# Kernel optimization log

Measured on AMD Instinct MI355X. Metric: run time of the kernel, lower is better.

## Reference

```python
import jax, jax.numpy as jnp
import numpy as np

N = 100000   # total nodes in batch
E = 200000   # total edges
G = 4000     # number of graphs
H = 128      # gin_size = gin_hidden = gin_mlp_hidden = linear_hidden
L = 2        # gin_layers


def setup_inputs() -> dict:
    key = jax.random.key(0)
    ks = jax.random.split(key, 24)
    rn = lambda i, shape, s=0.05: (jax.random.normal(ks[i], shape, jnp.float32) * s)
    inp = dict(
        x=rn(0, (N, 14), 1.0),
        edge_attr=rn(1, (E, 4), 1.0),
        edge_index=jax.random.randint(ks[2], (2, E), 0, N, dtype=jnp.int32),
        batch=jnp.sort(jax.random.randint(ks[3], (N,), 0, G, dtype=jnp.int32)),
        node_w=rn(4, (14, H)), node_b=jnp.zeros((H,), jnp.float32),
        edge_w=rn(5, (4, H)), edge_b=jnp.zeros((H,), jnp.float32),
        eps=jnp.zeros((L,), jnp.float32),
        gin_w1=rn(6, (L, H, H)), gin_b1=jnp.zeros((L, H), jnp.float32),
        gin_w2=rn(7, (L, H, H)), gin_b2=jnp.zeros((L, H), jnp.float32),
        em_w1=rn(8, (L, H, H)), em_b1=jnp.zeros((L, H), jnp.float32),
        em_w2=rn(9, (L, H, H)), em_b2=jnp.zeros((L, H), jnp.float32),
        gru_wih=rn(10, (3 * H, H)), gru_whh=rn(11, (3 * H, H)),
        gru_bih=jnp.zeros((3 * H,), jnp.float32), gru_bhh=jnp.zeros((3 * H,), jnp.float32),
        lstm_wih=rn(12, (4 * H, 2 * H)), lstm_whh=rn(13, (4 * H, H)),
        lstm_bih=jnp.zeros((4 * H,), jnp.float32), lstm_bhh=jnp.zeros((4 * H,), jnp.float32),
        fc_w1=rn(14, (2 * H, H)), fc_b1=jnp.zeros((H,), jnp.float32),
        fc_w2=rn(15, (H, 1)), fc_b2=jnp.zeros((1,), jnp.float32),
    )
    return inp


def reference(x, edge_attr, edge_index, batch,
              node_w, node_b, edge_w, edge_b, eps,
              gin_w1, gin_b1, gin_w2, gin_b2,
              em_w1, em_b1, em_w2, em_b2,
              gru_wih, gru_whh, gru_bih, gru_bhh,
              lstm_wih, lstm_whh, lstm_bih, lstm_bhh,
              fc_w1, fc_b1, fc_w2, fc_b2):
    src, dst = edge_index[0], edge_index[1]
    node = x @ node_w + node_b          # [N,H]
    edge = edge_attr @ edge_w + edge_b  # [E,H]
    h = node                            # GRU hidden state
    for l in range(L):
        # GINEConv: msg = relu(x_src + e), scatter-add to dst, (1+eps)*x + agg, then MLP
        msg = jax.nn.relu(node[src] + edge)                     # [E,H] gather
        agg = jax.ops.segment_sum(msg, dst, num_segments=N)     # [N,H] scatter-add
        z = (1.0 + eps[l]) * node + agg
        m = jax.nn.relu(z @ gin_w1[l] + gin_b1[l]) @ gin_w2[l] + gin_b2[l]
        # GRU cell (seq_len=1)
        gi = m @ gru_wih.T + gru_bih
        gh = h @ gru_whh.T + gru_bhh
        ir, iz, inn = jnp.split(gi, 3, axis=-1)
        hr, hz, hn = jnp.split(gh, 3, axis=-1)
        r = jax.nn.sigmoid(ir + hr)
        zt = jax.nn.sigmoid(iz + hz)
        n = jnp.tanh(inn + r * hn)
        h = (1.0 - zt) * n + zt * h
        node = h
        # edge feature update MLP
        edge = jax.nn.relu(edge @ em_w1[l] + em_b1[l]) @ em_w2[l] + em_b2[l]
    # Set2Set pooling, processing_steps=3
    qs = jnp.zeros((G, 2 * H), node.dtype)
    hl = jnp.zeros((G, H), node.dtype)
    cl = jnp.zeros((G, H), node.dtype)
    for _ in range(3):
        g = qs @ lstm_wih.T + lstm_bih + hl @ lstm_whh.T + lstm_bhh
        i_, f_, g_, o_ = jnp.split(g, 4, axis=-1)
        cl = jax.nn.sigmoid(f_) * cl + jax.nn.sigmoid(i_) * jnp.tanh(g_)
        hl = jax.nn.sigmoid(o_) * jnp.tanh(cl)
        q = hl                                                   # [G,H]
        e = jnp.sum(node * q[batch], axis=-1)                    # [N]
        emax = jax.ops.segment_max(e, batch, num_segments=G)
        ex = jnp.exp(e - emax[batch])
        denom = jax.ops.segment_sum(ex, batch, num_segments=G)
        a = ex / jnp.maximum(denom, 1e-9)[batch]                 # per-graph softmax
        r = jax.ops.segment_sum(a[:, None] * node, batch, num_segments=G)  # [G,H]
        qs = jnp.concatenate([q, r], axis=-1)                    # [G,2H]
    out = jax.nn.relu(qs @ fc_w1 + fc_b1) @ fc_w2 + fc_b2
    return out.reshape(-1)
```

## Files before the change

kernel.cpp:

```cpp
#include <hip/hip_runtime.h>
#include <hip/hip_bf16.h>

constexpr int TN = 100000;
constexpr int TE = 200000;
constexpr int TG = 4000;
constexpr int TH = 128;

using short8 = __attribute__((ext_vector_type(8))) short;
using f32x4  = __attribute__((ext_vector_type(4))) float;
typedef __hip_bfloat16 bf16;

#define DEVINL __device__ __forceinline__
DEVINL float sigm(float x)  { return 1.f / (1.f + __expf(-x)); }
DEVINL float ftanh(float x) { return 1.f - 2.f / (__expf(2.f * x) + 1.f); }
DEVINL void unpack8(uint4 v, float* f) {
    const ushort* u = (const ushort*)&v;
#pragma unroll
    for (int j = 0; j < 8; ++j) f[j] = __bfloat162float(*(const bf16*)&u[j]);
}

DEVINL void gload_lds16(const ushort* gsrc, ushort* ldst) {
    __builtin_amdgcn_global_load_lds(
        (const __attribute__((address_space(1))) void*)gsrc,
        (__attribute__((address_space(3))) void*)ldst, 16, 0, 0);
}

__global__ void convAll(const float* __restrict__ g1, const float* __restrict__ g2,
                        const float* __restrict__ e1, const float* __restrict__ e2,
                        const float* __restrict__ gwih, const float* __restrict__ gwhh,
                        const float* __restrict__ lwih, const float* __restrict__ lwhh,
                        bf16* __restrict__ w6, bf16* __restrict__ wgru,
                        bf16* __restrict__ wl) {
    int i = blockIdx.x * 256 + threadIdx.x;
    if (i < 6 * TH * TH) {
        int m = i >> 14, r = i & 16383;
        int n = r >> 7, k = r & 127;
        const float* s = (m == 0) ? g1 : (m == 1) ? g1 + TH * TH
                       : (m == 2) ? g2 : (m == 3) ? g2 + TH * TH
                       : (m == 4) ? e1 : e2;
        w6[i] = __float2bfloat16(s[k * TH + n]);
        return;
    }
    i -= 6 * TH * TH;
    if (i < 2 * 384 * TH) {
        const float* s = (i < 384 * TH) ? gwih : gwhh;
        int r = (i < 384 * TH) ? i : i - 384 * TH;
        wgru[i] = __float2bfloat16(s[r]);
        return;
    }
    i -= 2 * 384 * TH;
    if (i < 512 * 256) {
        int c = i >> 8, k = i & 255;
        float v = (k < 128) ? lwih[c * 256 + k] + lwhh[c * 128 + k] : lwih[c * 256 + k];
        wl[i] = __float2bfloat16(v);
    }
}

template<int K>
__global__ __launch_bounds__(256) void proj64(const float* __restrict__ X,
                                              const float* __restrict__ W,
                                              const float* __restrict__ b,
                                              ushort* __restrict__ out, int M) {
    __shared__ float xs[64][K];
    int tid = threadIdx.x;
    int bm = blockIdx.x * 64;
    for (int i = tid; i < 64 * K; i += 256) {
        int r = i / K, k = i % K;
        xs[r][k] = (bm + r < M) ? X[(size_t)(bm + r) * K + k] : 0.f;
    }
    __syncthreads();
    int rb = tid >> 4, h0 = (tid & 15) * 8;
    float acc[4][8];
#pragma unroll
    for (int j = 0; j < 4; ++j)
#pragma unroll
        for (int c = 0; c < 8; ++c) acc[j][c] = b[h0 + c];
#pragma unroll
    for (int k = 0; k < K; ++k) {
        float4 w0 = *(const float4*)(W + k * TH + h0);
        float4 w1 = *(const float4*)(W + k * TH + h0 + 4);
#pragma unroll
        for (int j = 0; j < 4; ++j) {
            float xv = xs[rb + 16 * j][k];
            acc[j][0] = fmaf(xv, w0.x, acc[j][0]); acc[j][1] = fmaf(xv, w0.y, acc[j][1]);
            acc[j][2] = fmaf(xv, w0.z, acc[j][2]); acc[j][3] = fmaf(xv, w0.w, acc[j][3]);
            acc[j][4] = fmaf(xv, w1.x, acc[j][4]); acc[j][5] = fmaf(xv, w1.y, acc[j][5]);
            acc[j][6] = fmaf(xv, w1.z, acc[j][6]); acc[j][7] = fmaf(xv, w1.w, acc[j][7]);
        }
    }
#pragma unroll
    for (int j = 0; j < 4; ++j) {
        int row = bm + rb + 16 * j;
        if (row >= M) continue;
        ushort o[8];
#pragma unroll
        for (int c = 0; c < 8; ++c) {
            bf16 v = __float2bfloat16(acc[j][c]);
            o[c] = *(ushort*)&v;
        }
        *(uint4*)(out + (size_t)row * TH + h0) = *(uint4*)o;
    }
}

__global__ __launch_bounds__(256) void proj_scatter(
    const float* __restrict__ X, const float* __restrict__ W,
    const float* __restrict__ b, const int* __restrict__ perm,
    ushort* __restrict__ out, int M) {
    __shared__ float xs[64][4];
    int tid = threadIdx.x;
    int bm = blockIdx.x * 64;
    if (tid < 64) {
        float4 a = make_float4(0.f, 0.f, 0.f, 0.f);
        if (bm + tid < M) a = *(const float4*)(X + (size_t)(bm + tid) * 4);
        xs[tid][0] = a.x; xs[tid][1] = a.y; xs[tid][2] = a.z; xs[tid][3] = a.w;
    }
    __syncthreads();
    int rb = tid >> 4, h0 = (tid & 15) * 8;
    float acc[4][8];
#pragma unroll
    for (int j = 0; j < 4; ++j)
#pragma unroll
        for (int c = 0; c < 8; ++c) acc[j][c] = b[h0 + c];
#pragma unroll
    for (int k = 0; k < 4; ++k) {
        float4 w0 = *(const float4*)(W + k * TH + h0);
        float4 w1 = *(const float4*)(W + k * TH + h0 + 4);
#pragma unroll
        for (int j = 0; j < 4; ++j) {
            float xv = xs[rb + 16 * j][k];
            acc[j][0] = fmaf(xv, w0.x, acc[j][0]); acc[j][1] = fmaf(xv, w0.y, acc[j][1]);
            acc[j][2] = fmaf(xv, w0.z, acc[j][2]); acc[j][3] = fmaf(xv, w0.w, acc[j][3]);
            acc[j][4] = fmaf(xv, w1.x, acc[j][4]); acc[j][5] = fmaf(xv, w1.y, acc[j][5]);
            acc[j][6] = fmaf(xv, w1.z, acc[j][6]); acc[j][7] = fmaf(xv, w1.w, acc[j][7]);
        }
    }
#pragma unroll
    for (int j = 0; j < 4; ++j) {
        int row = bm + rb + 16 * j;
        if (row >= M) continue;
        ushort o[8];
#pragma unroll
        for (int c = 0; c < 8; ++c) {
            bf16 v = __float2bfloat16(acc[j][c]);
            o[c] = *(ushort*)&v;
        }
        *(uint4*)(out + (size_t)perm[row] * TH + h0) = *(uint4*)o;
    }
}

__global__ void count_deg(const int* __restrict__ ei_dst, int* __restrict__ deg, int En) {
    int e = blockIdx.x * 256 + threadIdx.x;
    if (e < En) atomicAdd(&deg[ei_dst[e]], 1);
}
__global__ void scan_block(const int* __restrict__ deg, int* __restrict__ rowptr,
                           int* __restrict__ bsum, int Nn) {
    __shared__ int sm[256];
    int tid = threadIdx.x;
    int gid = blockIdx.x * 256 + tid;
    int v = (gid < Nn) ? deg[gid] : 0;
    int x = v;
    sm[tid] = x; __syncthreads();
    for (int off = 1; off < 256; off <<= 1) {
        int t = (tid >= off) ? sm[tid - off] : 0;
        __syncthreads();
        x += t; sm[tid] = x;
        __syncthreads();
    }
    if (gid < Nn) rowptr[gid] = x - v;
    if (tid == 255) bsum[blockIdx.x] = x;
}
__global__ void scan_bsum(const int* __restrict__ bsum, int* __restrict__ bsumx, int nb) {
    __shared__ int sm[512];
    int tid = threadIdx.x;
    int v = (tid < nb) ? bsum[tid] : 0;
    int x = v;
    sm[tid] = x; __syncthreads();
    for (int off = 1; off < 512; off <<= 1) {
        int t = (tid >= off) ? sm[tid - off] : 0;
        __syncthreads();
        x += t; sm[tid] = x;
        __syncthreads();
    }
    if (tid < nb) bsumx[tid] = x - v;
}
__global__ void add_off(int* __restrict__ rowptr, const int* __restrict__ bsumx,
                        int Nn, int Etot) {
    int gid = blockIdx.x * 256 + threadIdx.x;
    if (gid < Nn) rowptr[gid] += bsumx[gid >> 8];
    if (gid == 0) rowptr[Nn] = Etot;
}
__global__ void fill_csr(const int* __restrict__ ei_src, const int* __restrict__ ei_dst,
                         const int* __restrict__ rowptr, int* __restrict__ cur,
                         int* __restrict__ srcp, int* __restrict__ epos, int En) {
    int e = blockIdx.x * 256 + threadIdx.x;
    if (e >= En) return;
    int d = ei_dst[e];
    int p = atomicAdd(&cur[d], 1);
    int slot = rowptr[d] + p;
    srcp[slot] = ei_src[e];
    epos[e] = slot;
}
__global__ void build_gptr(const int* __restrict__ batch, int* __restrict__ gptr,
                           int Nn, int Gn) {
    int n = blockIdx.x * 256 + threadIdx.x;
    if (n >= Nn) return;
    int bc = batch[n];
    int bp = (n == 0) ? -1 : batch[n - 1];
    for (int g = bp + 1; g <= bc; ++g) gptr[g] = n;
    if (n == Nn - 1) for (int g = bc + 1; g <= Gn; ++g) gptr[g] = Nn;
}

__global__ __launch_bounds__(256) void aggregate_v8(
    const ushort* __restrict__ node, const ushort* __restrict__ ef,
    const int* __restrict__ srcp, const int* __restrict__ rowptr,
    const float* __restrict__ eps, int l, ushort* __restrict__ zb, int Nn) {
    int t = blockIdx.x * 256 + threadIdx.x;
    int n = t >> 4;
    if (n >= Nn) return;
    int c8 = (t & 15) * 8;
    float se = 1.f + eps[l];
    float acc[8];
    uint4 nv = *(const uint4*)(node + (size_t)n * TH + c8);
    unpack8(nv, acc);
#pragma unroll
    for (int j = 0; j < 8; ++j) acc[j] *= se;
    int s0 = rowptr[n], s1 = rowptr[n + 1];
    int i = s0;
    for (; i + 1 < s1; i += 2) {
        int sa = srcp[i], sb = srcp[i + 1];
        uint4 av0 = *(const uint4*)(node + (size_t)sa * TH + c8);
        uint4 bv0 = *(const uint4*)(ef + (size_t)i * TH + c8);
        uint4 av1 = *(const uint4*)(node + (size_t)sb * TH + c8);
        uint4 bv1 = *(const uint4*)(ef + (size_t)(i + 1) * TH + c8);
        float a0[8], b0[8], a1[8], b1[8];
        unpack8(av0, a0); unpack8(bv0, b0);
        unpack8(av1, a1); unpack8(bv1, b1);
#pragma unroll
        for (int j = 0; j < 8; ++j)
            acc[j] += fmaxf(a0[j] + b0[j], 0.f) + fmaxf(a1[j] + b1[j], 0.f);
    }
    if (i < s1) {
        int sa = srcp[i];
        uint4 av = *(const uint4*)(node + (size_t)sa * TH + c8);
        uint4 bv = *(const uint4*)(ef + (size_t)i * TH + c8);
        float af[8], bf[8];
        unpack8(av, af); unpack8(bv, bf);
#pragma unroll
        for (int j = 0; j < 8; ++j) acc[j] += fmaxf(af[j] + bf[j], 0.f);
    }
    ushort o[8];
#pragma unroll
    for (int j = 0; j < 8; ++j) {
        bf16 v = __float2bfloat16(acc[j]);
        o[j] = *(ushort*)&v;
    }
    *(uint4*)(zb + (size_t)n * TH + c8) = *(uint4*)o;
}

__global__ __launch_bounds__(256, 2) void mlp2_fused(
    const ushort* __restrict__ A, const ushort* __restrict__ W1t,
    const float* __restrict__ b1, const ushort* __restrict__ W2t,
    const float* __restrict__ b2, ushort* __restrict__ C, int M)
{
    __shared__ ushort As[128 * 128];
    const int tid = threadIdx.x;
    const int bm = blockIdx.x * 128;
    const int lane = tid & 63, w = tid >> 6;
    const int lr = lane & 15, lq = lane >> 4;
    const int wm = (w & 1) * 64, wn = (w >> 1) * 64;
    short8 wf[4][4];
#pragma unroll
    for (int ni = 0; ni < 4; ++ni)
#pragma unroll
        for (int ks = 0; ks < 4; ++ks)
            wf[ni][ks] = *(const short8*)(W1t + (size_t)(wn + ni * 16 + lr) * 128 + ks * 32 + lq * 8);
#pragma unroll
    for (int i = 0; i < 8; ++i) {
        int s = w * 512 + i * 64 + lane;
        int r = s >> 4;
        int c = (s & 15) ^ (r & 15);
        gload_lds16(A + (size_t)(bm + r) * 128 + c * 8, As + (w * 512 + i * 64) * 8);
    }
    __syncthreads();
    f32x4 acc[4][4] = {};
#pragma unroll
    for (int ks = 0; ks < 4; ++ks) {
        int cb = ks * 4 + lq;
        short8 af[4];
#pragma unroll
        for (int mi = 0; mi < 4; ++mi)
            af[mi] = *(const short8*)(&As[(wm + mi * 16 + lr) * 128 + ((cb ^ lr) * 8)]);
#pragma unroll
        for (int mi = 0; mi < 4; ++mi)
#pragma unroll
            for (int ni = 0; ni < 4; ++ni)
                acc[mi][ni] = __builtin_amdgcn_mfma_f32_16x16x32_bf16(af[mi], wf[ni][ks], acc[mi][ni], 0, 0, 0);
    }
    __syncthreads();
#pragma unroll
    for (int mi = 0; mi < 4; ++mi)
#pragma unroll
        for (int reg = 0; reg < 4; ++reg) {
            int row = wm + mi * 16 + lq * 4 + reg;
#pragma unroll
            for (int ni = 0; ni < 4; ++ni) {
                int col = wn + ni * 16 + lr;
                float v = fmaxf(acc[mi][ni][reg] + b1[col], 0.f);
                bf16 bv = __float2bfloat16(v);
                As[row * 128 + (((col >> 3) ^ (row & 15)) * 8) + (col & 7)] = *(ushort*)&bv;
            }
        }
#pragma unroll
    for (int ni = 0; ni < 4; ++ni)
#pragma unroll
        for (int ks = 0; ks < 4; ++ks)
            wf[ni][ks] = *(const short8*)(W2t + (size_t)(wn + ni * 16 + lr) * 128 + ks * 32 + lq * 8);
    __syncthreads();
    {
        f32x4 acc2[4][4] = {};
#pragma unroll
        for (int ks = 0; ks < 4; ++ks) {
            int cb = ks * 4 + lq;
            short8 af[4];
#pragma unroll
            for (int mi = 0; mi < 4; ++mi)
                af[mi] = *(const short8*)(&As[(wm + mi * 16 + lr) * 128 + ((cb ^ lr) * 8)]);
#pragma unroll
            for (int mi = 0; mi < 4; ++mi)
#pragma unroll
                for (int ni = 0; ni < 4; ++ni)
                    acc2[mi][ni] = __builtin_amdgcn_mfma_f32_16x16x32_bf16(af[mi], wf[ni][ks], acc2[mi][ni], 0, 0, 0);
        }
#pragma unroll
        for (int mi = 0; mi < 4; ++mi)
#pragma unroll
            for (int reg = 0; reg < 4; ++reg) {
                int row = bm + wm + mi * 16 + lq * 4 + reg;
                if (row >= M) continue;
#pragma unroll
                for (int ni = 0; ni < 4; ++ni) {
                    int col = wn + ni * 16 + lr;
                    bf16 bv = __float2bfloat16(acc2[mi][ni][reg] + b2[col]);
                    C[(size_t)row * 128 + col] = *(ushort*)&bv;
                }
            }
    }
}

__global__ __launch_bounds__(512, 2) void gru_fused(
    const ushort* __restrict__ mfeat, const ushort* __restrict__ wih,
    const ushort* __restrict__ whh, const float* __restrict__ bih,
    const float* __restrict__ bhh, ushort* __restrict__ node, int Nn, int nT)
{
    __shared__ ushort Ms[2][64 * 128];
    __shared__ ushort Hs[2][64 * 128];
    const int tid = threadIdx.x;
    const int lane = tid & 63, w = tid >> 6;
    const int lr = lane & 15, lq = lane >> 4;
    const int col = w * 16 + lr;
    short8 W[6][4];
#pragma unroll
    for (int ks = 0; ks < 4; ++ks) {
        int koff = ks * 32 + lq * 8;
        W[0][ks] = *(const short8*)(wih + (size_t)col * 128 + koff);
        W[1][ks] = *(const short8*)(wih + (size_t)(128 + col) * 128 + koff);
        W[2][ks] = *(const short8*)(wih + (size_t)(256 + col) * 128 + koff);
        W[3][ks] = *(const short8*)(whh + (size_t)col * 128 + koff);
        W[4][ks] = *(const short8*)(whh + (size_t)(128 + col) * 128 + koff);
        W[5][ks] = *(const short8*)(whh + (size_t)(256 + col) * 128 + koff);
    }
    const float br  = bih[col] + bhh[col];
    const float bz  = bih[128 + col] + bhh[128 + col];
    const float bin = bih[256 + col], bhn = bhh[256 + col];

    auto stage = [&](int tt, int buf) {
#pragma unroll
        for (int i = 0; i < 2; ++i) {
            int sb = w * 128 + i * 64;
            int s = sb + lane;
            int r = s >> 4;
            int c = (s & 15) ^ (r & 15);
            size_t goff = (size_t)(tt * 64 + r) * 128 + c * 8;
            gload_lds16(mfeat + goff, &Ms[buf][sb * 8]);
            gload_lds16(node + goff, &Hs[buf][sb * 8]);
        }
    };

    int t = blockIdx.x;
    const int G = gridDim.x;
    if (t >= nT) return;
    stage(t, 0);
    int cur = 0;
    while (t < nT) {
        int tn = t + G;
        if (tn < nT) {
            stage(tn, cur ^ 1);
            asm volatile("s_waitcnt vmcnt(4)" ::: "memory");
        } else {
            asm volatile("s_waitcnt vmcnt(0)" ::: "memory");
        }
        __builtin_amdgcn_sched_barrier(0);
        __builtin_amdgcn_s_barrier();
        __builtin_amdgcn_sched_barrier(0);
        {
            const ushort* Mc = Ms[cur];
            const ushort* Hc = Hs[cur];
            f32x4 aR[4] = {}, aZ[4] = {}, aN[4] = {}, aH[4] = {};
#pragma unroll
            for (int ks = 0; ks < 4; ++ks) {
                int cb = ks * 4 + lq;
#pragma unroll
                for (int rt = 0; rt < 4; ++rt) {
                    int off = (rt * 16 + lr) * 128 + ((cb ^ lr) * 8);
                    short8 am = *(const short8*)(&Mc[off]);
                    short8 ah = *(const short8*)(&Hc[off]);
                    aR[rt] = __builtin_amdgcn_mfma_f32_16x16x32_bf16(am, W[0][ks], aR[rt], 0, 0, 0);
                    aR[rt] = __builtin_amdgcn_mfma_f32_16x16x32_bf16(ah, W[3][ks], aR[rt], 0, 0, 0);
                    aZ[rt] = __builtin_amdgcn_mfma_f32_16x16x32_bf16(am, W[1][ks], aZ[rt], 0, 0, 0);
                    aZ[rt] = __builtin_amdgcn_mfma_f32_16x16x32_bf16(ah, W[4][ks], aZ[rt], 0, 0, 0);
                    aN[rt] = __builtin_amdgcn_mfma_f32_16x16x32_bf16(am, W[2][ks], aN[rt], 0, 0, 0);
                    aH[rt] = __builtin_amdgcn_mfma_f32_16x16x32_bf16(ah, W[5][ks], aH[rt], 0, 0, 0);
                }
            }
            const int bm = t * 64;
#pragma unroll
            for (int rt = 0; rt < 4; ++rt)
#pragma unroll
                for (int reg = 0; reg < 4; ++reg) {
                    int lrow = rt * 16 + lq * 4 + reg;
                    int row = bm + lrow;
                    if (row >= Nn) continue;
                    float r = sigm(aR[rt][reg] + br);
                    float z = sigm(aZ[rt][reg] + bz);
                    float n = ftanh(aN[rt][reg] + bin + r * (aH[rt][reg] + bhn));
                    int hofs = lrow * 128 + (((col >> 3) ^ (lrow & 15)) * 8) + (col & 7);
                    float hold = __bfloat162float(*(const bf16*)&Hc[hofs]);
                    bf16 hv = __float2bfloat16((1.f - z) * n + z * hold);
                    node[(size_t)row * 128 + col] = *(ushort*)&hv;
                }
        }
        __builtin_amdgcn_sched_barrier(0);
        __builtin_amdgcn_s_barrier();
        __builtin_amdgcn_sched_barrier(0);
        cur ^= 1;
        t = tn;
    }
}

__global__ __launch_bounds__(256) void lstm_fused(
    ushort* __restrict__ s, const ushort* __restrict__ Wl,
    const float* __restrict__ bih, const float* __restrict__ bhh,
    float* __restrict__ cl, int Gn)
{
    __shared__ ushort Ss[16 * 256];
    const int tid = threadIdx.x;
    const int bm = blockIdx.x * 16;
#pragma unroll
    for (int p = 0; p < 2; ++p) {
        int ch = p * 256 + tid;
        int r = ch >> 5, c = ch & 31;
        int row = bm + r;
        uint4 v = make_uint4(0u, 0u, 0u, 0u);
        if (row < Gn) v = *(const uint4*)(s + (size_t)row * 256 + c * 8);
        *(uint4*)(&Ss[r * 256 + ((c ^ (r & 15)) * 8)]) = v;
    }
    __syncthreads();
    const int lane = tid & 63, w = tid >> 6;
    const int lr = lane & 15, lq = lane >> 4;
    f32x4 acc[4][2] = {};
#pragma unroll
    for (int ks = 0; ks < 8; ++ks) {
        int cb = ks * 4 + lq;
        short8 am = *(const short8*)(&Ss[lr * 256 + ((cb ^ lr) * 8)]);
        int koff = ks * 32 + lq * 8;
#pragma unroll
        for (int g = 0; g < 4; ++g)
#pragma unroll
            for (int sub = 0; sub < 2; ++sub) {
                int col = g * 128 + w * 32 + sub * 16 + lr;
                short8 bf = *(const short8*)(Wl + (size_t)col * 256 + koff);
                acc[g][sub] = __builtin_amdgcn_mfma_f32_16x16x32_bf16(am, bf, acc[g][sub], 0, 0, 0);
            }
    }
#pragma unroll
    for (int sub = 0; sub < 2; ++sub) {
        int h = w * 32 + sub * 16 + lr;
        float bi = bih[h] + bhh[h];
        float bff = bih[128 + h] + bhh[128 + h];
        float bg = bih[256 + h] + bhh[256 + h];
        float bo = bih[384 + h] + bhh[384 + h];
#pragma unroll
        for (int reg = 0; reg < 4; ++reg) {
            int row = bm + lq * 4 + reg;
            if (row >= Gn) continue;
            float iv = sigm(acc[0][sub][reg] + bi);
            float fv = sigm(acc[1][sub][reg] + bff);
            float gv = ftanh(acc[2][sub][reg] + bg);
            float ov = sigm(acc[3][sub][reg] + bo);
            float c = fv * cl[(size_t)row * 128 + h] + iv * gv;
            cl[(size_t)row * 128 + h] = c;
            bf16 hv = __float2bfloat16(ov * ftanh(c));
            s[(size_t)row * 256 + h] = *(ushort*)&hv;
        }
    }
}

__global__ __launch_bounds__(256) void att_fused(
    const ushort* __restrict__ node, ushort* __restrict__ s,
    const int* __restrict__ gptr)
{
    __shared__ float q[128];
    __shared__ float es[512];
    __shared__ float red[8];
    __shared__ float part[16][128];
    int g = blockIdx.x;
    int tid = threadIdx.x, lane = tid & 63, wid = tid >> 6;
    int n0 = gptr[g], n1 = gptr[g + 1];
    int cnt = n1 - n0; if (cnt > 512) cnt = 512;
    if (tid < 128) q[tid] = __bfloat162float(((const bf16*)s)[(size_t)g * 256 + tid]);
    __syncthreads();
    int gr = tid >> 4, c8 = (tid & 15) * 8;
    for (int i0 = 0; i0 < cnt; i0 += 16) {
        int i = i0 + gr;
        float p = 0.f;
        if (i < cnt) {
            uint4 v = *(const uint4*)(node + (size_t)(n0 + i) * TH + c8);
            float f[8]; unpack8(v, f);
#pragma unroll
            for (int j = 0; j < 8; ++j) p = fmaf(f[j], q[c8 + j], p);
        }
        p += __shfl_down(p, 8, 16);
        p += __shfl_down(p, 4, 16);
        p += __shfl_down(p, 2, 16);
        p += __shfl_down(p, 1, 16);
        if ((tid & 15) == 0 && i < cnt) es[i] = p;
    }
    __syncthreads();
    float m = -1e30f;
    for (int i = tid; i < cnt; i += 256) m = fmaxf(m, es[i]);
    for (int off = 32; off; off >>= 1) m = fmaxf(m, __shfl_down(m, off));
    if (lane == 0) red[wid] = m;
    __syncthreads();
    m = fmaxf(fmaxf(red[0], red[1]), fmaxf(red[2], red[3]));
    float sm = 0.f;
    for (int i = tid; i < cnt; i += 256) { float ex = __expf(es[i] - m); es[i] = ex; sm += ex; }
    for (int off = 32; off; off >>= 1) sm += __shfl_down(sm, off);
    if (lane == 0) red[4 + wid] = sm;
    __syncthreads();
    sm = red[4] + red[5] + red[6] + red[7];
    float inv = 1.f / fmaxf(sm, 1e-9f);
    float racc[8] = {};
    for (int i = gr; i < cnt; i += 16) {
        uint4 v = *(const uint4*)(node + (size_t)(n0 + i) * TH + c8);
        float f[8]; unpack8(v, f);
        float a = es[i];
#pragma unroll
        for (int j = 0; j < 8; ++j) racc[j] = fmaf(a, f[j], racc[j]);
    }
#pragma unroll
    for (int j = 0; j < 8; ++j) part[gr][c8 + j] = racc[j];
    __syncthreads();
    if (tid < 128) {
        float r = 0.f;
#pragma unroll
        for (int k = 0; k < 16; ++k) r += part[k][tid];
        bf16 rv = __float2bfloat16(r * inv);
        s[(size_t)g * 256 + 128 + tid] = *(ushort*)&rv;
    }
}

__global__ __launch_bounds__(128) void final_fc(const ushort* __restrict__ s,
                                                const float* __restrict__ w1,
                                                const float* __restrict__ b1,
                                                const float* __restrict__ w2,
                                                const float* __restrict__ b2,
                                                float* __restrict__ out) {
    __shared__ float q[256];
    __shared__ float red[2];
    int g = blockIdx.x, t = threadIdx.x;
    q[t] = __bfloat162float(((const bf16*)s)[(size_t)g * 256 + t]);
    q[t + 128] = __bfloat162float(((const bf16*)s)[(size_t)g * 256 + 128 + t]);
    __syncthreads();
    float acc = b1[t];
    for (int k = 0; k < 256; ++k) acc = fmaf(q[k], w1[k * TH + t], acc);
    acc = fmaxf(acc, 0.f);
    float p = acc * w2[t];
    for (int off = 32; off; off >>= 1) p += __shfl_down(p, off);
    if ((t & 63) == 0) red[t >> 6] = p;
    __syncthreads();
    if (t == 0) out[g] = red[0] + red[1] + b2[0];
}

static void launch_mlp2(const void* A, const bf16* W1t, const float* b1,
                        const bf16* W2t, const float* b2, void* C, int M, hipStream_t s) {
    hipLaunchKernelGGL(mlp2_fused, dim3((M + 127) / 128), dim3(256), 0, s,
                       (const ushort*)A, (const ushort*)W1t, b1, (const ushort*)W2t, b2,
                       (ushort*)C, M);
}

extern "C" void kernel_launch(void* const* d_in, const int* in_sizes, int n_in,
                              void* d_out, int out_size, void* d_ws, size_t ws_size,
                              hipStream_t stream) {
    const float* x         = (const float*)d_in[0];
    const float* edge_attr = (const float*)d_in[1];
    const int*   edge_index= (const int*)d_in[2];
    const int*   batch     = (const int*)d_in[3];
    const float* node_w    = (const float*)d_in[4];
    const float* node_b    = (const float*)d_in[5];
    const float* edge_w    = (const float*)d_in[6];
    const float* edge_b    = (const float*)d_in[7];
    const float* eps       = (const float*)d_in[8];
    const float* gin_w1    = (const float*)d_in[9];
    const float* gin_b1    = (const float*)d_in[10];
    const float* gin_w2    = (const float*)d_in[11];
    const float* gin_b2    = (const float*)d_in[12];
    const float* em_w1     = (const float*)d_in[13];
    const float* em_b1     = (const float*)d_in[14];
    const float* em_w2     = (const float*)d_in[15];
    const float* em_b2     = (const float*)d_in[16];
    const float* gru_wih   = (const float*)d_in[17];
    const float* gru_whh   = (const float*)d_in[18];
    const float* gru_bih   = (const float*)d_in[19];
    const float* gru_bhh   = (const float*)d_in[20];
    const float* lstm_wih  = (const float*)d_in[21];
    const float* lstm_whh  = (const float*)d_in[22];
    const float* lstm_bih  = (const float*)d_in[23];
    const float* lstm_bhh  = (const float*)d_in[24];
    const float* fc_w1     = (const float*)d_in[25];
    const float* fc_b1     = (const float*)d_in[26];
    const float* fc_w2     = (const float*)d_in[27];
    const float* fc_b2     = (const float*)d_in[28];
    float* out = (float*)d_out;
    const int* ei_src = edge_index;
    const int* ei_dst = edge_index + TE;

    char* base = (char*)d_ws;
    size_t off = 0;
    auto alloc = [&](size_t bytes) { void* p = base + off; off += (bytes + 15) & ~size_t(15); return p; };
    bf16*  nodeb = (bf16*)alloc((size_t)TN * TH * 2);
    bf16*  zb    = (bf16*)alloc((size_t)TN * TH * 2);
    bf16*  e1b   = (bf16*)alloc((size_t)TE * TH * 2);
    int*   deg   = (int*)alloc((size_t)TN * 4);
    int*   rowptr= (int*)alloc((size_t)(TN + 1) * 4);
    int*   cur   = (int*)alloc((size_t)TN * 4);
    int*   srcp  = (int*)alloc((size_t)TE * 4);
    int*   epos  = (int*)alloc((size_t)TE * 4);
    int*   bsum  = (int*)alloc(512 * 4);
    int*   bsumx = (int*)alloc(512 * 4);
    int*   gptr  = (int*)alloc((size_t)(TG + 1) * 4);
    bf16*  w6    = (bf16*)alloc(6 * TH * TH * 2);
    bf16*  wgru  = (bf16*)alloc(2 * 384 * TH * 2);
    bf16*  wl    = (bf16*)alloc(512 * 256 * 2);
    if (ws_size < off) return;

    bf16* w_gin1_0 = w6;
    bf16* w_gin1_1 = w6 + 1 * TH * TH;
    bf16* w_gin2_0 = w6 + 2 * TH * TH;
    bf16* w_gin2_1 = w6 + 3 * TH * TH;
    bf16* w_em1    = w6 + 4 * TH * TH;
    bf16* w_em2    = w6 + 5 * TH * TH;
    bf16* w_wih    = wgru;
    bf16* w_whh    = wgru + 384 * TH;

    ushort* sbuf = (ushort*)e1b;
    float*  cl   = (float*)(sbuf + (size_t)TG * 256);

    hipMemsetAsync(deg, 0, (size_t)TN * 4, stream);
    hipMemsetAsync(cur, 0, (size_t)TN * 4, stream);
    count_deg<<<(TE + 255) / 256, 256, 0, stream>>>(ei_dst, deg, TE);
    int nb = (TN + 255) / 256;
    scan_block<<<nb, 256, 0, stream>>>(deg, rowptr, bsum, TN);
    scan_bsum<<<1, 512, 0, stream>>>(bsum, bsumx, nb);
    add_off<<<nb, 256, 0, stream>>>(rowptr, bsumx, TN, TE);
    fill_csr<<<(TE + 255) / 256, 256, 0, stream>>>(ei_src, ei_dst, rowptr, cur, srcp, epos, TE);
    build_gptr<<<(TN + 255) / 256, 256, 0, stream>>>(batch, gptr, TN, TG);

    int convTot = 6 * TH * TH + 2 * 384 * TH + 512 * 256;
    convAll<<<(convTot + 255) / 256, 256, 0, stream>>>(
        gin_w1, gin_w2, em_w1, em_w2, gru_wih, gru_whh, lstm_wih, lstm_whh,
        w6, wgru, wl);

    proj64<14><<<(TN + 63) / 64, 256, 0, stream>>>(x, node_w, node_b, (ushort*)nodeb, TN);
    proj_scatter<<<(TE + 63) / 64, 256, 0, stream>>>(edge_attr, edge_w, edge_b,
                                                     epos, (ushort*)e1b, TE);

    const int ntG = (TN + 63) / 64;

    aggregate_v8<<<(TN * 16 + 255) / 256, 256, 0, stream>>>(
        (const ushort*)nodeb, (const ushort*)e1b, srcp, rowptr, eps, 0, (ushort*)zb, TN);
    launch_mlp2(zb, w_gin1_0, gin_b1, w_gin2_0, gin_b2, zb, TN, stream);
    gru_fused<<<512, 512, 0, stream>>>(
        (const ushort*)zb, (const ushort*)w_wih, (const ushort*)w_whh,
        gru_bih, gru_bhh, (ushort*)nodeb, TN, ntG);

    launch_mlp2(e1b, w_em1, em_b1, w_em2, em_b2, e1b, TE, stream);
    aggregate_v8<<<(TN * 16 + 255) / 256, 256, 0, stream>>>(
        (const ushort*)nodeb, (const ushort*)e1b, srcp, rowptr, eps, 1, (ushort*)zb, TN);
    launch_mlp2(zb, w_gin1_1, gin_b1 + TH, w_gin2_1, gin_b2 + TH, zb, TN, stream);
    gru_fused<<<512, 512, 0, stream>>>(
        (const ushort*)zb, (const ushort*)w_wih, (const ushort*)w_whh,
        gru_bih, gru_bhh, (ushort*)nodeb, TN, ntG);

    hipMemsetAsync(sbuf, 0, (size_t)TG * 256 * 2 + (size_t)TG * 128 * 4, stream);
    for (int st = 0; st < 3; ++st) {
        lstm_fused<<<(TG + 15) / 16, 256, 0, stream>>>(
            sbuf, (const ushort*)wl, lstm_bih, lstm_bhh, cl, TG);
        att_fused<<<TG, 256, 0, stream>>>((const ushort*)nodeb, sbuf, gptr);
    }

    final_fc<<<TG, 128, 0, stream>>>(sbuf, fc_w1, fc_b1, fc_w2, fc_b2, out);
}
```

Before: 522.3 us.

## Fuse Set2Set LSTM, attention and final FC into one per-16-graph kernel

Merges the three-step Set2Set loop (LSTM gates, per-graph softmax attention, readout) and the final MLP into a single kernel in which each block owns 16 graphs and keeps q, r and the cell state in LDS. This removes seven launches, the memset and the global round-trips of the query and cell state. In exchange each graph is handled by only 16 threads that walk its nodes serially, and there are just 250 blocks, so parallelism in the attention phase drops sharply. The GRU kernel's grid is also halved from 512 to 256 blocks.

New measurement: 541.5 us. 1.04x slower.

```diff
diff --git a/kernel.cpp b/kernel.cpp
--- a/kernel.cpp
+++ b/kernel.cpp
@@ -447,148 +447,150 @@
     }
 }
 
-__global__ __launch_bounds__(256) void lstm_fused(
-    ushort* __restrict__ s, const ushort* __restrict__ Wl,
+__global__ __launch_bounds__(256) void set2set_fused(
+    const ushort* __restrict__ node, const ushort* __restrict__ Wl,
     const float* __restrict__ bih, const float* __restrict__ bhh,
-    float* __restrict__ cl, int Gn)
+    const int* __restrict__ gptr,
+    const float* __restrict__ w1, const float* __restrict__ b1,
+    const float* __restrict__ w2, const float* __restrict__ b2,
+    float* __restrict__ out, int Gn)
 {
-    __shared__ ushort Ss[16 * 256];
+    __shared__ ushort qsb[16 * 256];
+    __shared__ float  qf[16][128];
+    __shared__ float  rf[16][128];
+    __shared__ float  clb[16][128];
+    __shared__ float  es[16][512];
     const int tid = threadIdx.x;
     const int bm = blockIdx.x * 16;
-#pragma unroll
-    for (int p = 0; p < 2; ++p) {
-        int ch = p * 256 + tid;
-        int r = ch >> 5, c = ch & 31;
-        int row = bm + r;
-        uint4 v = make_uint4(0u, 0u, 0u, 0u);
-        if (row < Gn) v = *(const uint4*)(s + (size_t)row * 256 + c * 8);
-        *(uint4*)(&Ss[r * 256 + ((c ^ (r & 15)) * 8)]) = v;
+    for (int i = tid; i < 16 * 256; i += 256) qsb[i] = 0;
+    for (int i = tid; i < 16 * 128; i += 256) {
+        (&qf[0][0])[i] = 0.f;
+        (&clb[0][0])[i] = 0.f;
     }
     __syncthreads();
     const int lane = tid & 63, w = tid >> 6;
     const int lr = lane & 15, lq = lane >> 4;
-    f32x4 acc[4][2] = {};
-#pragma unroll
-    for (int ks = 0; ks < 8; ++ks) {
-        int cb = ks * 4 + lq;
-        short8 am = *(const short8*)(&Ss[lr * 256 + ((cb ^ lr) * 8)]);
-        int koff = ks * 32 + lq * 8;
-#pragma unroll
-        for (int g = 0; g < 4; ++g)
-#pragma unroll
-            for (int sub = 0; sub < 2; ++sub) {
-                int col = g * 128 + w * 32 + sub * 16 + lr;
-                short8 bf = *(const short8*)(Wl + (size_t)col * 256 + koff);
-                acc[g][sub] = __builtin_amdgcn_mfma_f32_16x16x32_bf16(am, bf, acc[g][sub], 0, 0, 0);
+    const int gi = tid >> 4, l16 = tid & 15;
+    const int g = bm + gi;
+    const bool live = g < Gn;
+    const int n0 = live ? gptr[g] : 0;
+    const int n1 = live ? gptr[g + 1] : 0;
+    int cnt = n1 - n0; if (cnt > 512) cnt = 512;
+
+    for (int step = 0; step < 3; ++step) {
+        f32x4 acc[4][2] = {};
+#pragma unroll
+        for (int ks = 0; ks < 8; ++ks) {
+            int cb = ks * 4 + lq;
+            short8 am = *(const short8*)(&qsb[lr * 256 + ((cb ^ lr) * 8)]);
+            int koff = ks * 32 + lq * 8;
+#pragma unroll
+            for (int gg = 0; gg < 4; ++gg)
+#pragma unroll
+                for (int sub = 0; sub < 2; ++sub) {
+                    int col = gg * 128 + w * 32 + sub * 16 + lr;
+                    short8 bf = *(const short8*)(Wl + (size_t)col * 256 + koff);
+                    acc[gg][sub] = __builtin_amdgcn_mfma_f32_16x16x32_bf16(am, bf, acc[gg][sub], 0, 0, 0);
+                }
+        }
+        __syncthreads();
+#pragma unroll
+        for (int sub = 0; sub < 2; ++sub) {
+            int h = w * 32 + sub * 16 + lr;
+            float bi = bih[h] + bhh[h];
+            float bff = bih[128 + h] + bhh[128 + h];
+            float bg = bih[256 + h] + bhh[256 + h];
+            float bo = bih[384 + h] + bhh[384 + h];
+#pragma unroll
+            for (int reg = 0; reg < 4; ++reg) {
+                int row = lq * 4 + reg;
+                float iv = sigm(acc[0][sub][reg] + bi);
+                float fv = sigm(acc[1][sub][reg] + bff);
+                float gv = ftanh(acc[2][sub][reg] + bg);
+                float ov = sigm(acc[3][sub][reg] + bo);
+                float c = fv * clb[row][h] + iv * gv;
+                clb[row][h] = c;
+                float hv = ov * ftanh(c);
+                qf[row][h] = hv;
+                bf16 hb = __float2bfloat16(hv);
+                qsb[row * 256 + (((h >> 3) ^ row) * 8) + (h & 7)] = *(ushort*)&hb;
             }
-    }
-#pragma unroll
-    for (int sub = 0; sub < 2; ++sub) {
-        int h = w * 32 + sub * 16 + lr;
-        float bi = bih[h] + bhh[h];
-        float bff = bih[128 + h] + bhh[128 + h];
-        float bg = bih[256 + h] + bhh[256 + h];
-        float bo = bih[384 + h] + bhh[384 + h];
-#pragma unroll
-        for (int reg = 0; reg < 4; ++reg) {
-            int row = bm + lq * 4 + reg;
-            if (row >= Gn) continue;
-            float iv = sigm(acc[0][sub][reg] + bi);
-            float fv = sigm(acc[1][sub][reg] + bff);
-            float gv = ftanh(acc[2][sub][reg] + bg);
-            float ov = sigm(acc[3][sub][reg] + bo);
-            float c = fv * cl[(size_t)row * 128 + h] + iv * gv;
-            cl[(size_t)row * 128 + h] = c;
-            bf16 hv = __float2bfloat16(ov * ftanh(c));
-            s[(size_t)row * 256 + h] = *(ushort*)&hv;
-        }
-    }
-}
-
-__global__ __launch_bounds__(256) void att_fused(
-    const ushort* __restrict__ node, ushort* __restrict__ s,
-    const int* __restrict__ gptr)
-{
-    __shared__ float q[128];
-    __shared__ float es[512];
-    __shared__ float red[8];
-    __shared__ float part[16][128];
-    int g = blockIdx.x;
-    int tid = threadIdx.x, lane = tid & 63, wid = tid >> 6;
-    int n0 = gptr[g], n1 = gptr[g + 1];
-    int cnt = n1 - n0; if (cnt > 512) cnt = 512;
-    if (tid < 128) q[tid] = __bfloat162float(((const bf16*)s)[(size_t)g * 256 + tid]);
-    __syncthreads();
-    int gr = tid >> 4, c8 = (tid & 15) * 8;
-    for (int i0 = 0; i0 < cnt; i0 += 16) {
-        int i = i0 + gr;
+        }
+        __syncthreads();
+        for (int i = 0; i < cnt; ++i) {
+            uint4 v = *(const uint4*)(node + (size_t)(n0 + i) * 128 + l16 * 8);
+            float f[8]; unpack8(v, f);
+            float p = 0.f;
+#pragma unroll
+            for (int j = 0; j < 8; ++j) p = fmaf(f[j], qf[gi][l16 * 8 + j], p);
+            p += __shfl_xor(p, 8, 16);
+            p += __shfl_xor(p, 4, 16);
+            p += __shfl_xor(p, 2, 16);
+            p += __shfl_xor(p, 1, 16);
+            if (l16 == 0) es[gi][i] = p;
+        }
+        float m = -1e30f;
+        for (int i = l16; i < cnt; i += 16) m = fmaxf(m, es[gi][i]);
+#pragma unroll
+        for (int off = 8; off; off >>= 1) m = fmaxf(m, __shfl_xor(m, off, 16));
+        float sm = 0.f;
+        for (int i = l16; i < cnt; i += 16) {
+            float ex = __expf(es[gi][i] - m);
+            es[gi][i] = ex;
+            sm += ex;
+        }
+#pragma unroll
+        for (int off = 8; off; off >>= 1) sm += __shfl_xor(sm, off, 16);
+        float inv = 1.f / fmaxf(sm, 1e-9f);
+        float racc[8] = {};
+        for (int i = 0; i < cnt; ++i) {
+            uint4 v = *(const uint4*)(node + (size_t)(n0 + i) * 128 + l16 * 8);
+            float f[8]; unpack8(v, f);
+            float a = es[gi][i];
+#pragma unroll
+            for (int j = 0; j < 8; ++j) racc[j] = fmaf(a, f[j], racc[j]);
+        }
+#pragma unroll
+        for (int j = 0; j < 8; ++j) {
+            int h = l16 * 8 + j;
+            float rv = racc[j] * inv;
+            rf[gi][h] = rv;
+            int h2 = 128 + h;
+            bf16 rb = __float2bfloat16(rv);
+            qsb[gi * 256 + (((h2 >> 3) ^ gi) * 8) + (h2 & 7)] = *(ushort*)&rb;
+        }
+        __syncthreads();
+    }
+    if (live) {
+        int h0 = l16 * 8;
+        float acch[8];
+#pragma unroll
+        for (int j = 0; j < 8; ++j) acch[j] = b1[h0 + j];
+        for (int k = 0; k < 128; ++k) {
+            float qk = qf[gi][k];
+            const float* wr = w1 + (size_t)k * 128 + h0;
+            float4 w0 = *(const float4*)wr, w4 = *(const float4*)(wr + 4);
+            acch[0] = fmaf(qk, w0.x, acch[0]); acch[1] = fmaf(qk, w0.y, acch[1]);
+            acch[2] = fmaf(qk, w0.z, acch[2]); acch[3] = fmaf(qk, w0.w, acch[3]);
+            acch[4] = fmaf(qk, w4.x, acch[4]); acch[5] = fmaf(qk, w4.y, acch[5]);
+            acch[6] = fmaf(qk, w4.z, acch[6]); acch[7] = fmaf(qk, w4.w, acch[7]);
+        }
+        for (int k = 0; k < 128; ++k) {
+            float qk = rf[gi][k];
+            const float* wr = w1 + (size_t)(128 + k) * 128 + h0;
+            float4 w0 = *(const float4*)wr, w4 = *(const float4*)(wr + 4);
+            acch[0] = fmaf(qk, w0.x, acch[0]); acch[1] = fmaf(qk, w0.y, acch[1]);
+            acch[2] = fmaf(qk, w0.z, acch[2]); acch[3] = fmaf(qk, w0.w, acch[3]);
+            acch[4] = fmaf(qk, w4.x, acch[4]); acch[5] = fmaf(qk, w4.y, acch[5]);
+            acch[6] = fmaf(qk, w4.z, acch[6]); acch[7] = fmaf(qk, w4.w, acch[7]);
+        }
         float p = 0.f;
-        if (i < cnt) {
-            uint4 v = *(const uint4*)(node + (size_t)(n0 + i) * TH + c8);
-            float f[8]; unpack8(v, f);
-#pragma unroll
-            for (int j = 0; j < 8; ++j) p = fmaf(f[j], q[c8 + j], p);
-        }
-        p += __shfl_down(p, 8, 16);
-        p += __shfl_down(p, 4, 16);
-        p += __shfl_down(p, 2, 16);
-        p += __shfl_down(p, 1, 16);
-        if ((tid & 15) == 0 && i < cnt) es[i] = p;
-    }
-    __syncthreads();
-    float m = -1e30f;
-    for (int i = tid; i < cnt; i += 256) m = fmaxf(m, es[i]);
-    for (int off = 32; off; off >>= 1) m = fmaxf(m, __shfl_down(m, off));
-    if (lane == 0) red[wid] = m;
-    __syncthreads();
-    m = fmaxf(fmaxf(red[0], red[1]), fmaxf(red[2], red[3]));
-    float sm = 0.f;
-    for (int i = tid; i < cnt; i += 256) { float ex = __expf(es[i] - m); es[i] = ex; sm += ex; }
-    for (int off = 32; off; off >>= 1) sm += __shfl_down(sm, off);
-    if (lane == 0) red[4 + wid] = sm;
-    __syncthreads();
-    sm = red[4] + red[5] + red[6] + red[7];
-    float inv = 1.f / fmaxf(sm, 1e-9f);
-    float racc[8] = {};
-    for (int i = gr; i < cnt; i += 16) {
-        uint4 v = *(const uint4*)(node + (size_t)(n0 + i) * TH + c8);
-        float f[8]; unpack8(v, f);
-        float a = es[i];
-#pragma unroll
-        for (int j = 0; j < 8; ++j) racc[j] = fmaf(a, f[j], racc[j]);
-    }
-#pragma unroll
-    for (int j = 0; j < 8; ++j) part[gr][c8 + j] = racc[j];
-    __syncthreads();
-    if (tid < 128) {
-        float r = 0.f;
-#pragma unroll
-        for (int k = 0; k < 16; ++k) r += part[k][tid];
-        bf16 rv = __float2bfloat16(r * inv);
-        s[(size_t)g * 256 + 128 + tid] = *(ushort*)&rv;
-    }
-}
-
-__global__ __launch_bounds__(128) void final_fc(const ushort* __restrict__ s,
-                                                const float* __restrict__ w1,
-                                                const float* __restrict__ b1,
-                                                const float* __restrict__ w2,
-                                                const float* __restrict__ b2,
-                                                float* __restrict__ out) {
-    __shared__ float q[256];
-    __shared__ float red[2];
-    int g = blockIdx.x, t = threadIdx.x;
-    q[t] = __bfloat162float(((const bf16*)s)[(size_t)g * 256 + t]);
-    q[t + 128] = __bfloat162float(((const bf16*)s)[(size_t)g * 256 + 128 + t]);
-    __syncthreads();
-    float acc = b1[t];
-    for (int k = 0; k < 256; ++k) acc = fmaf(q[k], w1[k * TH + t], acc);
-    acc = fmaxf(acc, 0.f);
-    float p = acc * w2[t];
-    for (int off = 32; off; off >>= 1) p += __shfl_down(p, off);
-    if ((t & 63) == 0) red[t >> 6] = p;
-    __syncthreads();
-    if (t == 0) out[g] = red[0] + red[1] + b2[0];
+#pragma unroll
+        for (int j = 0; j < 8; ++j) p += fmaxf(acch[j], 0.f) * w2[h0 + j];
+#pragma unroll
+        for (int off = 8; off; off >>= 1) p += __shfl_xor(p, off, 16);
+        if (l16 == 0) out[g] = p + b2[0];
+    }
 }
 
 static void launch_mlp2(const void* A, const bf16* W1t, const float* b1,
@@ -662,9 +664,6 @@
     bf16* w_wih    = wgru;
     bf16* w_whh    = wgru + 384 * TH;
 
-    ushort* sbuf = (ushort*)e1b;
-    float*  cl   = (float*)(sbuf + (size_t)TG * 256);
-
     hipMemsetAsync(deg, 0, (size_t)TN * 4, stream);
     hipMemsetAsync(cur, 0, (size_t)TN * 4, stream);
     count_deg<<<(TE + 255) / 256, 256, 0, stream>>>(ei_dst, deg, TE);
@@ -689,7 +688,7 @@
     aggregate_v8<<<(TN * 16 + 255) / 256, 256, 0, stream>>>(
         (const ushort*)nodeb, (const ushort*)e1b, srcp, rowptr, eps, 0, (ushort*)zb, TN);
     launch_mlp2(zb, w_gin1_0, gin_b1, w_gin2_0, gin_b2, zb, TN, stream);
-    gru_fused<<<512, 512, 0, stream>>>(
+    gru_fused<<<256, 512, 0, stream>>>(
         (const ushort*)zb, (const ushort*)w_wih, (const ushort*)w_whh,
         gru_bih, gru_bhh, (ushort*)nodeb, TN, ntG);
 
@@ -697,16 +696,11 @@
     aggregate_v8<<<(TN * 16 + 255) / 256, 256, 0, stream>>>(
         (const ushort*)nodeb, (const ushort*)e1b, srcp, rowptr, eps, 1, (ushort*)zb, TN);
     launch_mlp2(zb, w_gin1_1, gin_b1 + TH, w_gin2_1, gin_b2 + TH, zb, TN, stream);
-    gru_fused<<<512, 512, 0, stream>>>(
+    gru_fused<<<256, 512, 0, stream>>>(
         (const ushort*)zb, (const ushort*)w_wih, (const ushort*)w_whh,
         gru_bih, gru_bhh, (ushort*)nodeb, TN, ntG);
 
-    hipMemsetAsync(sbuf, 0, (size_t)TG * 256 * 2 + (size_t)TG * 128 * 4, stream);
-    for (int st = 0; st < 3; ++st) {
-        lstm_fused<<<(TG + 15) / 16, 256, 0, stream>>>(
-            sbuf, (const ushort*)wl, lstm_bih, lstm_bhh, cl, TG);
-        att_fused<<<TG, 256, 0, stream>>>((const ushort*)nodeb, sbuf, gptr);
-    }
-
-    final_fc<<<TG, 128, 0, stream>>>(sbuf, fc_w1, fc_b1, fc_w2, fc_b2, out);
-}
+    set2set_fused<<<(TG + 15) / 16, 256, 0, stream>>>(
+        (const ushort*)nodeb, (const ushort*)wl, lstm_bih, lstm_bhh, gptr,
+        fc_w1, fc_b1, fc_w2, fc_b2, out, TG);
+}
```
